# Kernel optimization log

Measured on AMD Instinct MI355X. Metric: run time of the kernel, lower is better.

Reference implementation:

```python
import jax, jax.numpy as jnp
import numpy as np

WBITS = 4   # weight bits (symmetric signed)
ABITS = 4   # activation bits (unsigned, [0,1])
CBITS = 4   # partial-sum quantization bits
ARRAY = 128 # crossbar array size (input-dim tile)
BN_EPS = 1e-5


def ste_round(x):
    # straight-through estimator round (identity gradient)
    return x + jax.lax.stop_gradient(jnp.round(x) - x)


def setup_inputs() -> dict:
    key = jax.random.key(0)
    k1, k2 = jax.random.split(key)
    B, FIN, FOUT = 65536, 256, 256
    x = jax.random.uniform(k1, (B, FIN), dtype=jnp.float32)        # quantized-act range [0,1]
    weight = jax.random.normal(k2, (FOUT, FIN), dtype=jnp.float32) * 0.05
    gamma = jnp.ones((FOUT,), jnp.float32)
    beta = jnp.zeros((FOUT,), jnp.float32)
    return {"x": x, "weight": weight, "gamma": gamma, "beta": beta}


def reference(x, weight, gamma, beta):
    qmax_w = 2 ** (WBITS - 1) - 1          # 7
    qmax_a = 2 ** ABITS - 1                # 15

    # --- symmetric weight quantization to WBITS (integer levels) ---
    scale_w = jnp.max(jnp.abs(weight)) / qmax_w
    w_int = ste_round(jnp.clip(weight / scale_w, -qmax_w, qmax_w))  # [Fout, Fin]

    # --- unsigned activation quantization to ABITS (integer levels) ---
    x_int = ste_round(jnp.clip(x, 0.0, 1.0) * qmax_a)               # [B, Fin]

    # --- crossbar-tiled integer matmul with partial-sum quantization ---
    B, Fin = x.shape
    Fout = weight.shape[0]
    T = Fin // ARRAY
    xt = x_int.reshape(B, T, ARRAY)          # [B, T, A]
    wt = w_int.reshape(Fout, T, ARRAY)       # [Fout, T, A]
    psum = jnp.einsum('bta,ota->bto', xt, wt)  # integer partial sums, [B, T, Fout]

    # quantize each partial sum to CBITS levels over the full tile dynamic range
    pmax = float(ARRAY * qmax_a * qmax_w)
    step = (2.0 * pmax) / (2 ** CBITS - 1)
    psum_q = ste_round(psum / step) * step

    acc = psum_q.sum(axis=1) * (scale_w / qmax_a)   # dequantized linear output [B, Fout]

    # --- BatchNorm1d (training mode: batch statistics) ---
    mu = acc.mean(axis=0)
    var = acc.var(axis=0)
    y = (acc - mu) * jax.lax.rsqrt(var + BN_EPS) * gamma + beta

    # --- quantized clipped-ReLU activation to ABITS ---
    out = ste_round(jnp.clip(y, 0.0, 1.0) * qmax_a) / qmax_a
    return out
```

## Files before the change

kernel.cpp:

```cpp
#include <hip/hip_runtime.h>
#include <cstdint>
#include <cstddef>

typedef int v4i __attribute__((ext_vector_type(4)));

static constexpr int NREP = 16;

static constexpr size_t WQ_OFF    = 0;
static constexpr size_t STATS_OFF = 65536;
static constexpr size_t SCALE_OFF = STATS_OFF + NREP*512*4;
static constexpr size_t AB_OFF    = SCALE_OFF + 64;
static constexpr size_t SBUF_OFF  = 131072;
static constexpr size_t WS_NEEDED = SBUF_OFF + (size_t)65536 * 256;

__device__ __forceinline__ int rhe1792(int p) {
    unsigned u = (unsigned)(p + 17024);
    unsigned v = u >> 8;
    unsigned d = (v * 147u) >> 10;
    int q = (int)d - 9;
    unsigned tie = (unsigned)((u & 255u) == 0u) & (unsigned)(v == 7u * d);
    q -= (int)(tie & ((unsigned)q & 1u));
    return q;
}

__global__ void k_zero(int* stats, unsigned* scalebits) {
    int idx = blockIdx.x * 256 + threadIdx.x;
    stats[idx] = 0;
    if (idx == 0) *scalebits = 0u;
}

__global__ void k_maxabs(const float* __restrict__ w, unsigned* scalebits) {
    int idx = blockIdx.x * 256 + threadIdx.x;
    float4 f = ((const float4*)w)[idx];
    float m = fmaxf(fmaxf(fabsf(f.x), fabsf(f.y)), fmaxf(fabsf(f.z), fabsf(f.w)));
    #pragma unroll
    for (int s = 32; s > 0; s >>= 1) m = fmaxf(m, __shfl_xor(m, s, 64));
    if ((threadIdx.x & 63) == 0) atomicMax(scalebits, __float_as_uint(m));
}

__global__ void k_wquant(const float* __restrict__ w, const unsigned* __restrict__ scalebits,
                         signed char* __restrict__ wq) {
    int idx = blockIdx.x * 256 + threadIdx.x;
    float scale = __uint_as_float(*scalebits) / 7.0f;
    float4 f = ((const float4*)w)[idx];
    int q0 = (int)rintf(fminf(fmaxf(f.x / scale, -7.f), 7.f));
    int q1 = (int)rintf(fminf(fmaxf(f.y / scale, -7.f), 7.f));
    int q2 = (int)rintf(fminf(fmaxf(f.z / scale, -7.f), 7.f));
    int q3 = (int)rintf(fminf(fmaxf(f.w / scale, -7.f), 7.f));
    ((int*)wq)[idx] = (q0 & 255) | ((q1 & 255) << 8) | ((q2 & 255) << 16) | ((q3 & 255) << 24);
}

template <typename ST>
__global__ __launch_bounds__(256, 3) void k_gemm(
    const float* __restrict__ x, const signed char* __restrict__ wq,
    ST* __restrict__ sbuf, int* __restrict__ stats)
{
    __shared__ __align__(16) signed char ldsx[2][16 * 272];
    const int tid  = threadIdx.x;
    const int lane = tid & 63;
    const int wv   = tid >> 6;
    const int obase = wv * 64;
    const int lr = lane & 15, quad = lane >> 4;

    v4i wf[4][4];
    #pragma unroll
    for (int ot = 0; ot < 4; ++ot)
        #pragma unroll
        for (int kt = 0; kt < 4; ++kt)
            wf[ot][kt] = *(const v4i*)(wq + (size_t)(obase + ot * 16 + lr) * 256 + kt * 64 + quad * 16);

    int ssum[4] = {0, 0, 0, 0};
    int ssq[4]  = {0, 0, 0, 0};

    const int r = tid >> 4, g = tid & 15;
    const int ITER = 4;
    const size_t rb0 = (size_t)blockIdx.x * (16 * ITER);

    float4 f[4];
    {
        const float4* xr = (const float4*)(x + (rb0 + r) * 256);
        #pragma unroll
        for (int j = 0; j < 4; ++j) f[j] = xr[j * 16 + g];
    }

    for (int it = 0; it < ITER; ++it) {
        signed char* lb = ldsx[it & 1];
        #pragma unroll
        for (int j = 0; j < 4; ++j) {
            int b0 = (int)rintf(fminf(fmaxf(f[j].x, 0.f), 1.f) * 15.f);
            int b1 = (int)rintf(fminf(fmaxf(f[j].y, 0.f), 1.f) * 15.f);
            int b2 = (int)rintf(fminf(fmaxf(f[j].z, 0.f), 1.f) * 15.f);
            int b3 = (int)rintf(fminf(fmaxf(f[j].w, 0.f), 1.f) * 15.f);
            *(int*)(lb + r * 272 + j * 64 + g * 4) = b0 | (b1 << 8) | (b2 << 16) | (b3 << 24);
        }
        __syncthreads();
        if (it + 1 < ITER) {
            const float4* xr = (const float4*)(x + (rb0 + (it + 1) * 16 + r) * 256);
            #pragma unroll
            for (int j = 0; j < 4; ++j) f[j] = xr[j * 16 + g];
        }
        v4i a[4];
        #pragma unroll
        for (int kt = 0; kt < 4; ++kt)
            a[kt] = *(const v4i*)(lb + lr * 272 + kt * 64 + quad * 16);
        const size_t rowbase = rb0 + (size_t)it * 16;
        #pragma unroll
        for (int ot = 0; ot < 4; ++ot) {
            v4i acc0 = {0, 0, 0, 0}, acc1 = {0, 0, 0, 0};
            acc0 = __builtin_amdgcn_mfma_i32_16x16x64_i8(a[0], wf[ot][0], acc0, 0, 0, 0);
            acc0 = __builtin_amdgcn_mfma_i32_16x16x64_i8(a[1], wf[ot][1], acc0, 0, 0, 0);
            acc1 = __builtin_amdgcn_mfma_i32_16x16x64_i8(a[2], wf[ot][2], acc1, 0, 0, 0);
            acc1 = __builtin_amdgcn_mfma_i32_16x16x64_i8(a[3], wf[ot][3], acc1, 0, 0, 0);
            const int ocol = obase + ot * 16 + lr;
            ST* sp = sbuf + (rowbase + quad * 4) * 256 + ocol;
            #pragma unroll
            for (int e = 0; e < 4; ++e) {
                int s = rhe1792(acc0[e]) + rhe1792(acc1[e]);
                ssum[ot] += s;
                ssq[ot]  += s * s;
                sp[(size_t)e * 256] = (ST)s;
            }
        }
    }
    int* st = stats + (blockIdx.x & (NREP - 1)) * 512;
    #pragma unroll
    for (int ot = 0; ot < 4; ++ot) {
        int v = ssum[ot], u = ssq[ot];
        v += __shfl_xor(v, 16, 64); v += __shfl_xor(v, 32, 64);
        u += __shfl_xor(u, 16, 64); u += __shfl_xor(u, 32, 64);
        if (quad == 0) {
            atomicAdd(&st[obase + ot * 16 + lr], v);
            atomicAdd(&st[256 + obase + ot * 16 + lr], u);
        }
    }
}

__global__ void k_stats(const int* __restrict__ stats, const unsigned* __restrict__ scalebits,
                        const float* __restrict__ gamma, const float* __restrict__ beta,
                        float2* __restrict__ AB)
{
    int o = threadIdx.x;
    int s = 0, q = 0;
    #pragma unroll
    for (int rr = 0; rr < NREP; ++rr) {
        s += stats[rr * 512 + o];
        q += stats[rr * 512 + 256 + o];
    }
    float scale_w = __uint_as_float(*scalebits) / 7.0f;
    float t = scale_w / 15.0f;
    double Cs = 1792.0 * (double)t;
    const double N = 65536.0;
    double mean_s = (double)s / N;
    double var_s  = (double)q / N - mean_s * mean_s;
    double var    = Cs * Cs * var_s;
    double inv    = 1.0 / sqrt(var + 1e-5);
    double A = Cs * inv * (double)gamma[o];
    double B = (double)beta[o] - Cs * mean_s * inv * (double)gamma[o];
    AB[o] = make_float2((float)A, (float)B);
}

template <typename LT>
__global__ __launch_bounds__(256) void k_out(const LT* sbuf, const float2* __restrict__ AB,
                                             float* out)
{
    __shared__ float2 ab[256];
    int tid = threadIdx.x;
    ab[tid] = AB[tid];
    __syncthreads();
    size_t base = ((size_t)blockIdx.x * 256 + tid) * 16;
    int o0 = (tid & 15) * 16;
    float vals[16];
    if constexpr (sizeof(LT) == 1) {
        v4i sv = *(const v4i*)((const signed char*)sbuf + base);
        #pragma unroll
        for (int j = 0; j < 4; ++j)
            #pragma unroll
            for (int e = 0; e < 4; ++e)
                vals[j * 4 + e] = (float)((sv[j] << (24 - 8 * e)) >> 24);
    } else {
        #pragma unroll
        for (int j = 0; j < 4; ++j) {
            float4 fl = ((const float4*)(sbuf + base))[j];
            vals[j * 4 + 0] = fl.x; vals[j * 4 + 1] = fl.y;
            vals[j * 4 + 2] = fl.z; vals[j * 4 + 3] = fl.w;
        }
    }
    #pragma unroll
    for (int m = 0; m < 16; ++m) {
        float2 t = ab[o0 + m];
        float y = vals[m] * t.x + t.y;
        y = fminf(fmaxf(y, 0.f), 1.f) * 15.f;
        vals[m] = rintf(y) * 0.066666666666666666f;
    }
    float4* op = (float4*)(out + base);
    #pragma unroll
    for (int j = 0; j < 4; ++j)
        op[j] = make_float4(vals[j * 4], vals[j * 4 + 1], vals[j * 4 + 2], vals[j * 4 + 3]);
}

extern "C" void kernel_launch(void* const* d_in, const int* in_sizes, int n_in,
                              void* d_out, int out_size, void* d_ws, size_t ws_size,
                              hipStream_t stream)
{
    const float* x     = (const float*)d_in[0];
    const float* w     = (const float*)d_in[1];
    const float* gamma = (const float*)d_in[2];
    const float* beta  = (const float*)d_in[3];
    float* out = (float*)d_out;
    char* ws = (char*)d_ws;

    signed char* wq        = (signed char*)(ws + WQ_OFF);
    int*         stats     = (int*)(ws + STATS_OFF);
    unsigned*    scalebits = (unsigned*)(ws + SCALE_OFF);
    float2*      AB        = (float2*)(ws + AB_OFF);

    k_zero<<<dim3(32), dim3(256), 0, stream>>>(stats, scalebits);
    k_maxabs<<<dim3(64), dim3(256), 0, stream>>>(w, scalebits);
    k_wquant<<<dim3(64), dim3(256), 0, stream>>>(w, scalebits, wq);

    if (ws_size >= WS_NEEDED) {
        signed char* sbuf = (signed char*)(ws + SBUF_OFF);
        k_gemm<signed char><<<dim3(1024), dim3(256), 0, stream>>>(x, wq, sbuf, stats);
        k_stats<<<dim3(1), dim3(256), 0, stream>>>(stats, scalebits, gamma, beta, AB);
        k_out<signed char><<<dim3(4096), dim3(256), 0, stream>>>(sbuf, AB, out);
    } else {
        k_gemm<float><<<dim3(1024), dim3(256), 0, stream>>>(x, wq, out, stats);
        k_stats<<<dim3(1), dim3(256), 0, stream>>>(stats, scalebits, gamma, beta, AB);
        k_out<float><<<dim3(4096), dim3(256), 0, stream>>>(out, AB, out);
    }
}
```

Before: 153.5 us.

## Use nontemporal loads/stores, coalesce k_out, replace zero kernel with memset

Loads of x in the GEMM and stores of the output in k_out now use nontemporal builtins so streaming traffic does not pollute the caches. k_out is restructured so that each thread handles one float4 per iteration at a stride of 256, giving coalesced accesses, and it reads its BN coefficients straight from global memory instead of staging them in LDS behind a barrier. The k_zero kernel is replaced by hipMemsetAsync. The rounding tie test is also simplified to a single comparison. A memset can carry its own launch overhead, and the nontemporal hints may do nothing on this hardware.

```diff
diff --git a/kernel.cpp b/kernel.cpp
--- a/kernel.cpp
+++ b/kernel.cpp
@@ -2,7 +2,8 @@
 #include <cstdint>
 #include <cstddef>
 
-typedef int v4i __attribute__((ext_vector_type(4)));
+typedef int   v4i __attribute__((ext_vector_type(4)));
+typedef float v4f __attribute__((ext_vector_type(4)));
 
 static constexpr int NREP = 16;
 
@@ -10,23 +11,18 @@
 static constexpr size_t STATS_OFF = 65536;
 static constexpr size_t SCALE_OFF = STATS_OFF + NREP*512*4;
 static constexpr size_t AB_OFF    = SCALE_OFF + 64;
-static constexpr size_t SBUF_OFF  = 131072;
+static constexpr size_t SBUF_OFF  = 131072 + 2048;
 static constexpr size_t WS_NEEDED = SBUF_OFF + (size_t)65536 * 256;
+static constexpr size_t ZERO_BYTES = NREP*512*4 + 64;
 
 __device__ __forceinline__ int rhe1792(int p) {
     unsigned u = (unsigned)(p + 17024);
     unsigned v = u >> 8;
     unsigned d = (v * 147u) >> 10;
     int q = (int)d - 9;
-    unsigned tie = (unsigned)((u & 255u) == 0u) & (unsigned)(v == 7u * d);
+    unsigned tie = (unsigned)(((u & 255u) | (v - 7u * d)) == 0u);
     q -= (int)(tie & ((unsigned)q & 1u));
     return q;
-}
-
-__global__ void k_zero(int* stats, unsigned* scalebits) {
-    int idx = blockIdx.x * 256 + threadIdx.x;
-    stats[idx] = 0;
-    if (idx == 0) *scalebits = 0u;
 }
 
 __global__ void k_maxabs(const float* __restrict__ w, unsigned* scalebits) {
@@ -76,28 +72,28 @@
     const int ITER = 4;
     const size_t rb0 = (size_t)blockIdx.x * (16 * ITER);
 
-    float4 f[4];
+    v4f f[4];
     {
-        const float4* xr = (const float4*)(x + (rb0 + r) * 256);
-        #pragma unroll
-        for (int j = 0; j < 4; ++j) f[j] = xr[j * 16 + g];
+        const v4f* xr = (const v4f*)(x + (rb0 + r) * 256);
+        #pragma unroll
+        for (int j = 0; j < 4; ++j) f[j] = __builtin_nontemporal_load(&xr[j * 16 + g]);
     }
 
     for (int it = 0; it < ITER; ++it) {
         signed char* lb = ldsx[it & 1];
         #pragma unroll
         for (int j = 0; j < 4; ++j) {
-            int b0 = (int)rintf(fminf(fmaxf(f[j].x, 0.f), 1.f) * 15.f);
-            int b1 = (int)rintf(fminf(fmaxf(f[j].y, 0.f), 1.f) * 15.f);
-            int b2 = (int)rintf(fminf(fmaxf(f[j].z, 0.f), 1.f) * 15.f);
-            int b3 = (int)rintf(fminf(fmaxf(f[j].w, 0.f), 1.f) * 15.f);
+            int b0 = (int)rintf(fminf(fmaxf(f[j][0], 0.f), 1.f) * 15.f);
+            int b1 = (int)rintf(fminf(fmaxf(f[j][1], 0.f), 1.f) * 15.f);
+            int b2 = (int)rintf(fminf(fmaxf(f[j][2], 0.f), 1.f) * 15.f);
+            int b3 = (int)rintf(fminf(fmaxf(f[j][3], 0.f), 1.f) * 15.f);
             *(int*)(lb + r * 272 + j * 64 + g * 4) = b0 | (b1 << 8) | (b2 << 16) | (b3 << 24);
         }
         __syncthreads();
         if (it + 1 < ITER) {
-            const float4* xr = (const float4*)(x + (rb0 + (it + 1) * 16 + r) * 256);
+            const v4f* xr = (const v4f*)(x + (rb0 + (it + 1) * 16 + r) * 256);
             #pragma unroll
-            for (int j = 0; j < 4; ++j) f[j] = xr[j * 16 + g];
+            for (int j = 0; j < 4; ++j) f[j] = __builtin_nontemporal_load(&xr[j * 16 + g]);
         }
         v4i a[4];
         #pragma unroll
@@ -163,39 +159,33 @@
 __global__ __launch_bounds__(256) void k_out(const LT* sbuf, const float2* __restrict__ AB,
                                              float* out)
 {
-    __shared__ float2 ab[256];
-    int tid = threadIdx.x;
-    ab[tid] = AB[tid];
-    __syncthreads();
-    size_t base = ((size_t)blockIdx.x * 256 + tid) * 16;
-    int o0 = (tid & 15) * 16;
-    float vals[16];
-    if constexpr (sizeof(LT) == 1) {
-        v4i sv = *(const v4i*)((const signed char*)sbuf + base);
-        #pragma unroll
-        for (int j = 0; j < 4; ++j)
-            #pragma unroll
-            for (int e = 0; e < 4; ++e)
-                vals[j * 4 + e] = (float)((sv[j] << (24 - 8 * e)) >> 24);
-    } else {
-        #pragma unroll
-        for (int j = 0; j < 4; ++j) {
-            float4 fl = ((const float4*)(sbuf + base))[j];
-            vals[j * 4 + 0] = fl.x; vals[j * 4 + 1] = fl.y;
-            vals[j * 4 + 2] = fl.z; vals[j * 4 + 3] = fl.w;
-        }
-    }
-    #pragma unroll
-    for (int m = 0; m < 16; ++m) {
-        float2 t = ab[o0 + m];
-        float y = vals[m] * t.x + t.y;
-        y = fminf(fmaxf(y, 0.f), 1.f) * 15.f;
-        vals[m] = rintf(y) * 0.066666666666666666f;
-    }
-    float4* op = (float4*)(out + base);
-    #pragma unroll
-    for (int j = 0; j < 4; ++j)
-        op[j] = make_float4(vals[j * 4], vals[j * 4 + 1], vals[j * 4 + 2], vals[j * 4 + 3]);
+    const int tid = threadIdx.x;
+    const int o0 = (tid * 4) & 255;
+    const float4 ab01 = *(const float4*)((const float*)AB + 2 * o0);
+    const float4 ab23 = *(const float4*)((const float*)AB + 2 * o0 + 4);
+    const size_t base = (size_t)blockIdx.x * 1024 + tid;
+    #pragma unroll
+    for (int j = 0; j < 4; ++j) {
+        const size_t F4 = base + (size_t)j * 256;
+        float v0, v1, v2, v3;
+        if constexpr (sizeof(LT) == 1) {
+            int sv = ((const int*)sbuf)[F4];
+            v0 = (float)((sv << 24) >> 24);
+            v1 = (float)((sv << 16) >> 24);
+            v2 = (float)((sv << 8) >> 24);
+            v3 = (float)(sv >> 24);
+        } else {
+            v4f fl = ((const v4f*)sbuf)[F4];
+            v0 = fl[0]; v1 = fl[1]; v2 = fl[2]; v3 = fl[3];
+        }
+        float y0 = rintf(fminf(fmaxf(v0 * ab01.x + ab01.y, 0.f), 1.f) * 15.f);
+        float y1 = rintf(fminf(fmaxf(v1 * ab01.z + ab01.w, 0.f), 1.f) * 15.f);
+        float y2 = rintf(fminf(fmaxf(v2 * ab23.x + ab23.y, 0.f), 1.f) * 15.f);
+        float y3 = rintf(fminf(fmaxf(v3 * ab23.z + ab23.w, 0.f), 1.f) * 15.f);
+        const float inv15 = 0.066666666666666666f;
+        v4f o = { y0 * inv15, y1 * inv15, y2 * inv15, y3 * inv15 };
+        __builtin_nontemporal_store(o, (v4f*)out + F4);
+    }
 }
 
 extern "C" void kernel_launch(void* const* d_in, const int* in_sizes, int n_in,
@@ -214,7 +204,7 @@
     unsigned*    scalebits = (unsigned*)(ws + SCALE_OFF);
     float2*      AB        = (float2*)(ws + AB_OFF);
 
-    k_zero<<<dim3(32), dim3(256), 0, stream>>>(stats, scalebits);
+    hipMemsetAsync(ws + STATS_OFF, 0, ZERO_BYTES, stream);
     k_maxabs<<<dim3(64), dim3(256), 0, stream>>>(w, scalebits);
     k_wquant<<<dim3(64), dim3(256), 0, stream>>>(w, scalebits, wq);
 
```

Measured after the change: 146.4 us. -4.6%, faster.
